# Kernel optimization log

Hardware: AMD Instinct MI355X
Metric: run time of the kernel (lower is better)

## Reference

```python
import jax, jax.numpy as jnp
import numpy as np

T, INPUT, POP_EXC, POP_INH = 128, 2048, 2048, 512
DT = 1e-3
TAU_SYN_INV, TAU_MEM_INV = 200.0, 100.0
V_LEAK, V_TH, V_RESET = 0.0, 1.0, 0.0
RHO_RESET = 5.0            # refractory counter reset (in steps)
ALPHA = 100.0              # SuperSpike surrogate slope (used in bwd variant)
A_PRE = A_POST = 1.0
TAU_PRE_INV = TAU_POST_INV = 50.0
ETA_PLUS = ETA_MINUS = 1e-3
W_MIN, W_MAX = 0.0, 1.0


def heaviside(x):
    return (x > 0).astype(x.dtype)


def lif_refrac_step(inp, v, i, rho):
    # norse LIF feed-forward step
    v_dec = v + DT * TAU_MEM_INV * ((V_LEAK - v) + i)
    i_dec = i * (1.0 - DT * TAU_SYN_INV)
    z = heaviside(v_dec - V_TH)
    v_new = (1.0 - z) * v_dec + z * V_RESET
    i_new = i_dec + inp
    # refractory update
    refrac = heaviside(rho)                      # neurons still refractory
    v_new = (1.0 - refrac) * v_new + refrac * V_RESET
    z = (1.0 - refrac) * z
    rho_new = (1.0 - z) * jax.nn.relu(rho - refrac) + z * RHO_RESET
    return z, v_new, i_new, rho_new


def stdp_step(z_pre, z_post, w, t_pre, t_post):
    # additive STDP (norse stdp_step_linear, mu=0) with trace low-pass filters
    t_pre = t_pre + DT * TAU_PRE_INV * (-t_pre + A_PRE * z_pre)
    t_post = t_post + DT * TAU_POST_INV * (-t_post + A_POST * z_post)
    dw = ETA_PLUS * jnp.outer(z_post, t_pre) - ETA_MINUS * jnp.outer(t_post, z_pre)
    w = jnp.clip(w + dw, W_MIN, W_MAX)           # (post, pre)
    return w, t_pre, t_post


def setup_inputs() -> dict:
    key = jax.random.key(0)
    k1, k2, k3 = jax.random.split(key, 3)
    exc_currents = 2.0 * jax.random.uniform(k1, (T, INPUT), dtype=jnp.float32)
    w_exc = 0.05 * jax.random.uniform(k2, (POP_EXC, INPUT), dtype=jnp.float32)
    w_inh = 0.05 * jax.random.uniform(k3, (POP_INH, POP_EXC), dtype=jnp.float32)
    return {"exc_currents": exc_currents, "w_exc": w_exc, "w_inh": w_inh}


def reference(exc_currents, w_exc, w_inh):
    zf = jnp.zeros
    carry0 = (
        w_exc, zf(POP_EXC), zf(POP_EXC), zf(POP_EXC),   # w, v, i, rho (exc)
        zf(INPUT), zf(POP_EXC),                         # t_pre, t_post (exc)
        w_inh, zf(POP_INH), zf(POP_INH), zf(POP_INH),   # w, v, i, rho (inh)
        zf(POP_EXC), zf(POP_INH),                       # t_pre, t_post (inh)
    )

    def step(c, x):
        (we, ve, ie, re, tpe, tqe, wi, vi, ii, ri, tpi, tqi) = c
        # excitatory STDP layer: matvec input current, LIF-refrac, STDP update
        z_e, ve, ie, re = lif_refrac_step(x @ we.T, ve, ie, re)
        we, tpe, tqe = stdp_step(x, z_e, we, tpe, tqe)
        # inhibitory STDP layer driven by excitatory spikes
        z_i, vi, ii, ri = lif_refrac_step(z_e @ wi.T, vi, ii, ri)
        wi, tpi, tqi = stdp_step(z_e, z_i, wi, tpi, tqi)
        return (we, ve, ie, re, tpe, tqe, wi, vi, ii, ri, tpi, tqi), z_e

    _, spikes = jax.lax.scan(step, carry0, exc_currents)
    return spikes  # [T, POP_EXC]
```

## Files before the change

kernel.cpp:

```cpp
#include <hip/hip_runtime.h>


constexpr int T_STEPS = 128;
constexpr int N_IN    = 2048;
constexpr int N_EXC   = 2048;

__global__ __launch_bounds__(256)
void tp_precompute_kernel(const float* __restrict__ x, float* __restrict__ tp_ws) {
    const int j = blockIdx.x * blockDim.x + threadIdx.x;
    float tp = 0.f;
    #pragma unroll 4
    for (int t = 0; t < T_STEPS; ++t) {
        tp = fmaf(0.05f, x[t * N_IN + j] - tp, tp);
        tp_ws[t * N_IN + j] = tp;
    }
}

template <int CTRL, int RM>
__device__ __forceinline__ float dpp_add(float x) {
    int t = __builtin_amdgcn_update_dpp(0, __builtin_bit_cast(int, x),
                                        CTRL, RM, 0xF, true);
    return x + __builtin_bit_cast(float, t);
}

__device__ __forceinline__ float wave_sum64(float x) {
    x = dpp_add<0x111, 0xF>(x);
    x = dpp_add<0x112, 0xF>(x);
    x = dpp_add<0x114, 0xF>(x);
    x = dpp_add<0x118, 0xF>(x);
    x = dpp_add<0x142, 0xA>(x);
    x = dpp_add<0x143, 0xC>(x);
    return __builtin_bit_cast(float,
        __builtin_amdgcn_readlane(__builtin_bit_cast(int, x), 63));
}

__device__ __forceinline__ float clamp01(float x) {
    return __builtin_amdgcn_fmed3f(x, 0.f, 1.f);
}

__global__ __launch_bounds__(256, 2)
void snn_exc_kernel(const float* __restrict__ x,
                    const float* __restrict__ w0,
                    const float* __restrict__ tp_ws,
                    float* __restrict__ out)
{
    __shared__ __align__(16) float xs[2][N_IN];

    const int tid  = threadIdx.x;
    const int lane = tid & 63;
    const int wid  = tid >> 6;
    const int row  = blockIdx.x * 4 + wid;

    float w[32];
    {
        const float4* wrow = reinterpret_cast<const float4*>(w0 + (size_t)row * N_IN);
        #pragma unroll
        for (int m = 0; m < 8; ++m) {
            float4 t4 = wrow[m * 64 + lane];
            w[4*m+0] = t4.x; w[4*m+1] = t4.y; w[4*m+2] = t4.z; w[4*m+3] = t4.w;
        }
    }

    const int stage_f = wid * 512 + lane * 4;
    const float4* tpb = reinterpret_cast<const float4*>(tp_ws) + lane;
    float* outp = out + row;

    {
        const float* s0 = x + stage_f;
        *reinterpret_cast<float4*>(&xs[0][stage_f])       = *reinterpret_cast<const float4*>(s0);
        *reinterpret_cast<float4*>(&xs[0][stage_f + 256]) = *reinterpret_cast<const float4*>(s0 + 256);
    }
    float4 pr0, pr1;
    {
        const float* s1 = x + N_IN + stage_f;
        pr0 = *reinterpret_cast<const float4*>(s1);
        pr1 = *reinterpret_cast<const float4*>(s1 + 256);
    }
    __syncthreads();

    float v = 0.f, syn = 0.f, rho = 0.f, tpost = 0.f;

    for (int t = 0; t < T_STEPS; ++t) {
        float4 xq[8];
        {
            const float4* xl = reinterpret_cast<const float4*>(xs[t & 1]);
            #pragma unroll
            for (int m = 0; m < 8; ++m) xq[m] = xl[m * 64 + lane];
        }

        {
            float* d = &xs[(t + 1) & 1][stage_f];
            *reinterpret_cast<float4*>(d)       = pr0;
            *reinterpret_cast<float4*>(d + 256) = pr1;
        }

        __syncthreads();

        {
            int tn = t + 2; if (tn > T_STEPS - 1) tn = T_STEPS - 1;
            const float* s = x + (size_t)tn * N_IN + stage_f;
            pr0 = *reinterpret_cast<const float4*>(s);
            pr1 = *reinterpret_cast<const float4*>(s + 256);
        }

        const float v_dec = fmaf(0.1f, syn - v, v);
        const bool refrac = (rho > 0.f);
        const bool spike  = (v_dec > 1.0f) && !refrac;
        v   = (spike || refrac) ? 0.f : v_dec;
        rho = spike ? 5.0f : fmaxf(rho - 1.0f, 0.f);
        const float zf = spike ? 1.f : 0.f;
        tpost = fmaf(0.05f, zf - tpost, tpost);
        const float c2 = 1e-3f * tpost;
        if (lane == 0) *outp = zf;
        outp += N_EXC;

        float4 tq[8];
        if (spike) {
            const float4* tq4 = tpb + (size_t)t * (N_IN / 4);
            #pragma unroll
            for (int m = 0; m < 8; ++m) tq[m] = tq4[m * 64];
        }

        float a0 = 0.f, a1 = 0.f, a2 = 0.f, a3 = 0.f;
        #pragma unroll
        for (int m = 0; m < 8; ++m) {
            a0 = fmaf(xq[m].x, w[4*m+0], a0);
            a1 = fmaf(xq[m].y, w[4*m+1], a1);
            a2 = fmaf(xq[m].z, w[4*m+2], a2);
            a3 = fmaf(xq[m].w, w[4*m+3], a3);
        }

        if (spike) {
            #pragma unroll
            for (int m = 0; m < 8; ++m) {
                w[4*m+0] = clamp01(fmaf(1e-3f, tq[m].x, fmaf(-c2, xq[m].x, w[4*m+0])));
                w[4*m+1] = clamp01(fmaf(1e-3f, tq[m].y, fmaf(-c2, xq[m].y, w[4*m+1])));
                w[4*m+2] = clamp01(fmaf(1e-3f, tq[m].z, fmaf(-c2, xq[m].z, w[4*m+2])));
                w[4*m+3] = clamp01(fmaf(1e-3f, tq[m].w, fmaf(-c2, xq[m].w, w[4*m+3])));
            }
        } else {
            #pragma unroll
            for (int m = 0; m < 8; ++m) {
                w[4*m+0] = clamp01(fmaf(-c2, xq[m].x, w[4*m+0]));
                w[4*m+1] = clamp01(fmaf(-c2, xq[m].y, w[4*m+1]));
                w[4*m+2] = clamp01(fmaf(-c2, xq[m].z, w[4*m+2]));
                w[4*m+3] = clamp01(fmaf(-c2, xq[m].w, w[4*m+3]));
            }
        }

        syn = fmaf(0.8f, syn, wave_sum64((a0 + a1) + (a2 + a3)));
    }
}

extern "C" void kernel_launch(void* const* d_in, const int* in_sizes, int n_in,
                              void* d_out, int out_size, void* d_ws, size_t ws_size,
                              hipStream_t stream) {
    const float* x  = (const float*)d_in[0];
    const float* w0 = (const float*)d_in[1];
    float* out = (float*)d_out;

    float* tp_ws = (float*)d_ws;
    tp_precompute_kernel<<<N_IN / 256, 256, 0, stream>>>(x, tp_ws);

    dim3 grid(N_EXC / 4);
    dim3 block(256);
    snn_exc_kernel<<<grid, block, 0, stream>>>(x, w0, tp_ws, out);
}
```

Before: 93.33 us.

## Process two neuron rows per wavefront to reuse staged input across rows

Each wavefront now keeps two weight rows in registers and computes both rows' matvec, LIF update and STDP update against the same shared-memory input vector. The grid is halved, so each timestep's LDS staging and barrier are shared by twice as many rows. Spike branches are made wave-uniform with readfirstlane, and the trace vector is loaded inside the branch. In exchange, register use roughly doubles, the launch bound drops to one block per CU, and there are only 256 blocks, which may leave parts of the GPU idle. The precompute loop unroll factor is also raised.

Measured after the change: 133.8 us. +43.3%, slower.

```diff
diff --git a/kernel.cpp b/kernel.cpp
--- a/kernel.cpp
+++ b/kernel.cpp
@@ -9,7 +9,7 @@
 void tp_precompute_kernel(const float* __restrict__ x, float* __restrict__ tp_ws) {
     const int j = blockIdx.x * blockDim.x + threadIdx.x;
     float tp = 0.f;
-    #pragma unroll 4
+    #pragma unroll 16
     for (int t = 0; t < T_STEPS; ++t) {
         tp = fmaf(0.05f, x[t * N_IN + j] - tp, tp);
         tp_ws[t * N_IN + j] = tp;
@@ -38,7 +38,7 @@
     return __builtin_amdgcn_fmed3f(x, 0.f, 1.f);
 }
 
-__global__ __launch_bounds__(256, 2)
+__global__ __launch_bounds__(256, 1)
 void snn_exc_kernel(const float* __restrict__ x,
                     const float* __restrict__ w0,
                     const float* __restrict__ tp_ws,
@@ -49,21 +49,24 @@
     const int tid  = threadIdx.x;
     const int lane = tid & 63;
     const int wid  = tid >> 6;
-    const int row  = blockIdx.x * 4 + wid;
-
-    float w[32];
+    const int rowA = blockIdx.x * 8 + wid * 2;
+
+    float wA[32], wB[32];
     {
-        const float4* wrow = reinterpret_cast<const float4*>(w0 + (size_t)row * N_IN);
+        const float4* ra = reinterpret_cast<const float4*>(w0 + (size_t)rowA * N_IN);
+        const float4* rb = reinterpret_cast<const float4*>(w0 + (size_t)(rowA + 1) * N_IN);
         #pragma unroll
         for (int m = 0; m < 8; ++m) {
-            float4 t4 = wrow[m * 64 + lane];
-            w[4*m+0] = t4.x; w[4*m+1] = t4.y; w[4*m+2] = t4.z; w[4*m+3] = t4.w;
+            float4 a = ra[m * 64 + lane];
+            float4 b = rb[m * 64 + lane];
+            wA[4*m+0] = a.x; wA[4*m+1] = a.y; wA[4*m+2] = a.z; wA[4*m+3] = a.w;
+            wB[4*m+0] = b.x; wB[4*m+1] = b.y; wB[4*m+2] = b.z; wB[4*m+3] = b.w;
         }
     }
 
     const int stage_f = wid * 512 + lane * 4;
-    const float4* tpb = reinterpret_cast<const float4*>(tp_ws) + lane;
-    float* outp = out + row;
+    float* outpA = out + rowA;
+    float* outpB = out + rowA + 1;
 
     {
         const float* s0 = x + stage_f;
@@ -78,7 +81,8 @@
     }
     __syncthreads();
 
-    float v = 0.f, syn = 0.f, rho = 0.f, tpost = 0.f;
+    float vA = 0.f, synA = 0.f, rhoA = 0.f, tpostA = 0.f;
+    float vB = 0.f, synB = 0.f, rhoB = 0.f, tpostB = 0.f;
 
     for (int t = 0; t < T_STEPS; ++t) {
         float4 xq[8];
@@ -93,7 +97,6 @@
             *reinterpret_cast<float4*>(d)       = pr0;
             *reinterpret_cast<float4*>(d + 256) = pr1;
         }
-
         __syncthreads();
 
         {
@@ -103,52 +106,84 @@
             pr1 = *reinterpret_cast<const float4*>(s + 256);
         }
 
-        const float v_dec = fmaf(0.1f, syn - v, v);
-        const bool refrac = (rho > 0.f);
-        const bool spike  = (v_dec > 1.0f) && !refrac;
-        v   = (spike || refrac) ? 0.f : v_dec;
-        rho = spike ? 5.0f : fmaxf(rho - 1.0f, 0.f);
-        const float zf = spike ? 1.f : 0.f;
-        tpost = fmaf(0.05f, zf - tpost, tpost);
-        const float c2 = 1e-3f * tpost;
-        if (lane == 0) *outp = zf;
-        outp += N_EXC;
-
-        float4 tq[8];
-        if (spike) {
-            const float4* tq4 = tpb + (size_t)t * (N_IN / 4);
-            #pragma unroll
-            for (int m = 0; m < 8; ++m) tq[m] = tq4[m * 64];
-        }
+        const float vdA = fmaf(0.1f, synA - vA, vA);
+        const bool  rfA = (rhoA > 0.f);
+        const bool  skA = (vdA > 1.0f) && !rfA;
+        vA    = (skA || rfA) ? 0.f : vdA;
+        rhoA  = skA ? 5.0f : fmaxf(rhoA - 1.0f, 0.f);
+        const float zA = skA ? 1.f : 0.f;
+        tpostA = fmaf(0.05f, zA - tpostA, tpostA);
+        const float c2A = 1e-3f * tpostA;
+
+        const float vdB = fmaf(0.1f, synB - vB, vB);
+        const bool  rfB = (rhoB > 0.f);
+        const bool  skB = (vdB > 1.0f) && !rfB;
+        vB    = (skB || rfB) ? 0.f : vdB;
+        rhoB  = skB ? 5.0f : fmaxf(rhoB - 1.0f, 0.f);
+        const float zB = skB ? 1.f : 0.f;
+        tpostB = fmaf(0.05f, zB - tpostB, tpostB);
+        const float c2B = 1e-3f * tpostB;
+
+        if (lane == 0) { *outpA = zA; *outpB = zB; }
+        outpA += N_EXC; outpB += N_EXC;
 
         float a0 = 0.f, a1 = 0.f, a2 = 0.f, a3 = 0.f;
+        float b0 = 0.f, b1 = 0.f, b2 = 0.f, b3 = 0.f;
         #pragma unroll
         for (int m = 0; m < 8; ++m) {
-            a0 = fmaf(xq[m].x, w[4*m+0], a0);
-            a1 = fmaf(xq[m].y, w[4*m+1], a1);
-            a2 = fmaf(xq[m].z, w[4*m+2], a2);
-            a3 = fmaf(xq[m].w, w[4*m+3], a3);
-        }
-
-        if (spike) {
-            #pragma unroll
-            for (int m = 0; m < 8; ++m) {
-                w[4*m+0] = clamp01(fmaf(1e-3f, tq[m].x, fmaf(-c2, xq[m].x, w[4*m+0])));
-                w[4*m+1] = clamp01(fmaf(1e-3f, tq[m].y, fmaf(-c2, xq[m].y, w[4*m+1])));
-                w[4*m+2] = clamp01(fmaf(1e-3f, tq[m].z, fmaf(-c2, xq[m].z, w[4*m+2])));
-                w[4*m+3] = clamp01(fmaf(1e-3f, tq[m].w, fmaf(-c2, xq[m].w, w[4*m+3])));
+            a0 = fmaf(xq[m].x, wA[4*m+0], a0);
+            b0 = fmaf(xq[m].x, wB[4*m+0], b0);
+            a1 = fmaf(xq[m].y, wA[4*m+1], a1);
+            b1 = fmaf(xq[m].y, wB[4*m+1], b1);
+            a2 = fmaf(xq[m].z, wA[4*m+2], a2);
+            b2 = fmaf(xq[m].z, wB[4*m+2], b2);
+            a3 = fmaf(xq[m].w, wA[4*m+3], a3);
+            b3 = fmaf(xq[m].w, wB[4*m+3], b3);
+        }
+
+        const int sAu = __builtin_amdgcn_readfirstlane((int)skA);
+        const int sBu = __builtin_amdgcn_readfirstlane((int)skB);
+        const float4* tq4 = reinterpret_cast<const float4*>(tp_ws + (size_t)t * N_IN) + lane;
+
+        if (sAu) {
+            #pragma unroll
+            for (int m = 0; m < 8; ++m) {
+                float4 tq = tq4[m * 64];
+                wA[4*m+0] = clamp01(fmaf(1e-3f, tq.x, fmaf(-c2A, xq[m].x, wA[4*m+0])));
+                wA[4*m+1] = clamp01(fmaf(1e-3f, tq.y, fmaf(-c2A, xq[m].y, wA[4*m+1])));
+                wA[4*m+2] = clamp01(fmaf(1e-3f, tq.z, fmaf(-c2A, xq[m].z, wA[4*m+2])));
+                wA[4*m+3] = clamp01(fmaf(1e-3f, tq.w, fmaf(-c2A, xq[m].w, wA[4*m+3])));
             }
         } else {
             #pragma unroll
             for (int m = 0; m < 8; ++m) {
-                w[4*m+0] = clamp01(fmaf(-c2, xq[m].x, w[4*m+0]));
-                w[4*m+1] = clamp01(fmaf(-c2, xq[m].y, w[4*m+1]));
-                w[4*m+2] = clamp01(fmaf(-c2, xq[m].z, w[4*m+2]));
-                w[4*m+3] = clamp01(fmaf(-c2, xq[m].w, w[4*m+3]));
-            }
-        }
-
-        syn = fmaf(0.8f, syn, wave_sum64((a0 + a1) + (a2 + a3)));
+                wA[4*m+0] = clamp01(fmaf(-c2A, xq[m].x, wA[4*m+0]));
+                wA[4*m+1] = clamp01(fmaf(-c2A, xq[m].y, wA[4*m+1]));
+                wA[4*m+2] = clamp01(fmaf(-c2A, xq[m].z, wA[4*m+2]));
+                wA[4*m+3] = clamp01(fmaf(-c2A, xq[m].w, wA[4*m+3]));
+            }
+        }
+        if (sBu) {
+            #pragma unroll
+            for (int m = 0; m < 8; ++m) {
+                float4 tq = tq4[m * 64];
+                wB[4*m+0] = clamp01(fmaf(1e-3f, tq.x, fmaf(-c2B, xq[m].x, wB[4*m+0])));
+                wB[4*m+1] = clamp01(fmaf(1e-3f, tq.y, fmaf(-c2B, xq[m].y, wB[4*m+1])));
+                wB[4*m+2] = clamp01(fmaf(1e-3f, tq.z, fmaf(-c2B, xq[m].z, wB[4*m+2])));
+                wB[4*m+3] = clamp01(fmaf(1e-3f, tq.w, fmaf(-c2B, xq[m].w, wB[4*m+3])));
+            }
+        } else {
+            #pragma unroll
+            for (int m = 0; m < 8; ++m) {
+                wB[4*m+0] = clamp01(fmaf(-c2B, xq[m].x, wB[4*m+0]));
+                wB[4*m+1] = clamp01(fmaf(-c2B, xq[m].y, wB[4*m+1]));
+                wB[4*m+2] = clamp01(fmaf(-c2B, xq[m].z, wB[4*m+2]));
+                wB[4*m+3] = clamp01(fmaf(-c2B, xq[m].w, wB[4*m+3]));
+            }
+        }
+
+        synA = fmaf(0.8f, synA, wave_sum64((a0 + a1) + (a2 + a3)));
+        synB = fmaf(0.8f, synB, wave_sum64((b0 + b1) + (b2 + b3)));
     }
 }
 
@@ -162,7 +197,7 @@
     float* tp_ws = (float*)d_ws;
     tp_precompute_kernel<<<N_IN / 256, 256, 0, stream>>>(x, tp_ws);
 
-    dim3 grid(N_EXC / 4);
+    dim3 grid(N_EXC / 8);
     dim3 block(256);
     snn_exc_kernel<<<grid, block, 0, stream>>>(x, w0, tp_ws, out);
 }
```
